# Optimization experiments

Hardware: AMD Instinct MI355X
Metric: run time of the kernel (lower is better)

## Reference

```python
import jax, jax.numpy as jnp
import numpy as np


def setup_inputs() -> dict:
    key = jax.random.key(0)
    ks = jax.random.split(key, 7)
    B, S, D, F, E = 4, 2048, 1024, 4096, 8
    scale = 0.02
    return {
        "x": jax.random.normal(ks[0], (B, S, D), dtype=jnp.float32),
        "gate_w": jax.random.normal(ks[1], (D, E), dtype=jnp.float32) * scale,
        "gate_b": jnp.zeros((E,), dtype=jnp.float32),
        "w1": jax.random.normal(ks[2], (E, D, F), dtype=jnp.float32) * scale,
        "b1": jnp.zeros((E, F), dtype=jnp.float32),
        "w2": jax.random.normal(ks[3], (E, F, D), dtype=jnp.float32) * scale,
        "b2": jnp.zeros((E, D), dtype=jnp.float32),
        "top_k": 2,
    }


def reference(x, gate_w, gate_b, w1, b1, w2, b2, top_k):
    B, S, D = x.shape
    E = w1.shape[0]
    xf = x.reshape(-1, D)                      # [T, D], T = B*S
    T = xf.shape[0]

    # Router: top-k logits, softmax over the selected k (as in torch code)
    logits = xf @ gate_w + gate_b              # [T, E]
    rw, sel = jax.lax.top_k(logits, top_k)     # [T, k], [T, k]
    w = jax.nn.softmax(rw, axis=-1)            # [T, k]

    # Dense combine weights: combine[t, e] = sum_k w[t,k] * (sel[t,k]==e)
    combine = jnp.zeros((T, E), dtype=xf.dtype)
    combine = combine.at[jnp.arange(T)[:, None], sel].add(w)

    # Loop over small fixed expert count; each expert FFN on all tokens,
    # weighted by combine (zero for unrouted tokens). Dropout p honored as 0 (eval).
    out = jnp.zeros_like(xf)
    for e in range(E):
        h = jax.nn.gelu(xf @ w1[e] + b1[e], approximate=False)  # torch F.gelu = exact
        out = out + combine[:, e:e + 1] * (h @ w2[e] + b2[e])
    return out.reshape(B, S, D)
```

## Files before the change

### kernel.cpp

```cpp
#include <hip/hip_runtime.h>
#include <math.h>

#define T_TOK 8192
#define DDIM  1024
#define FDIM  4096
#define NEXP  8
#define MT256 72
#define NSLOT (2 * T_TOK)
#define NG1   (16 * MT256)
#define NG2   (8 * MT256)

typedef __attribute__((ext_vector_type(8))) short short8;
typedef __attribute__((ext_vector_type(4))) float f32x4;
typedef unsigned short u16;
typedef unsigned int   u32;

typedef const __attribute__((address_space(1))) u32* gp_t;
typedef       __attribute__((address_space(3))) u32* lp_t;

__device__ __forceinline__ void gload16(const void* g, void* l) {
  __builtin_amdgcn_global_load_lds((gp_t)g, (lp_t)l, 16, 0, 0);
}

#define VM2 asm volatile("s_waitcnt vmcnt(2)" ::: "memory")
#define VM0 asm volatile("s_waitcnt vmcnt(0)" ::: "memory")
#define SBAR __builtin_amdgcn_s_barrier()
#define SCHED0 __builtin_amdgcn_sched_barrier(0)

__device__ __forceinline__ u16 f2bf(float f) {
  u32 u = __float_as_uint(f);
  u = u + 0x7FFFu + ((u >> 16) & 1u);
  return (u16)(u >> 16);
}

__device__ __forceinline__ int imin(int a, int b) { return a < b ? a : b; }

__device__ __forceinline__ float gelu_fast(float v) {
  float u = 0.7978845608f * (v + 0.044715f * v * v * v);
  float t2 = __expf(2.f * u);
  float th = 1.f - 2.f / (t2 + 1.f);
  return 0.5f * v * (1.f + th);
}

__device__ __forceinline__ int xcd_swz(int orig, int nwg) {
  int xcd = orig & 7;
  int q = nwg >> 3, r = nwg & 7;
  int base = (xcd < r) ? xcd * (q + 1) : r * (q + 1) + (xcd - r) * q;
  return base + (orig >> 3);
}

__global__ __launch_bounds__(256) void router_kernel(
    const float* __restrict__ x, const float* __restrict__ gw,
    const float* __restrict__ gb,
    int* __restrict__ counts, int* __restrict__ sel, float* __restrict__ wts)
{
  const int t    = blockIdx.x * 4 + (threadIdx.x >> 6);
  const int lane = threadIdx.x & 63;
  const float* xr = x + (size_t)t * DDIM;
  float lg[NEXP];
  #pragma unroll
  for (int e = 0; e < NEXP; e++) lg[e] = 0.f;
  #pragma unroll
  for (int i = 0; i < 4; i++) {
    int d0 = i * 256 + lane * 4;
    float4 v = *(const float4*)(xr + d0);
    const float* g = gw + (size_t)d0 * NEXP;
    #pragma unroll
    for (int e = 0; e < NEXP; e++)
      lg[e] += v.x * g[e] + v.y * g[NEXP + e] + v.z * g[2 * NEXP + e] + v.w * g[3 * NEXP + e];
  }
  #pragma unroll
  for (int off = 32; off > 0; off >>= 1) {
    #pragma unroll
    for (int e = 0; e < NEXP; e++) lg[e] += __shfl_down(lg[e], off);
  }
  if (lane == 0) {
    float v0 = -1e30f, v1 = -1e30f; int s0 = 0, s1 = 0;
    #pragma unroll
    for (int e = 0; e < NEXP; e++) {
      float v = lg[e] + gb[e];
      if (v > v0) { v1 = v0; s1 = s0; v0 = v; s0 = e; }
      else if (v > v1) { v1 = v; s1 = e; }
    }
    float a  = expf(v1 - v0);
    float w0 = 1.f / (1.f + a);
    sel[t * 2] = s0; sel[t * 2 + 1] = s1;
    wts[t * 2] = w0; wts[t * 2 + 1] = 1.f - w0;
    atomicAdd(&counts[s0], 1); atomicAdd(&counts[s1], 1);
  }
}

__global__ __launch_bounds__(256) void scan_assign_kernel(
    const int* __restrict__ counts, const int* __restrict__ sel,
    const float* __restrict__ wts,
    int* __restrict__ offsets, int* __restrict__ map_e, int* __restrict__ map_r,
    int* __restrict__ nT, int* __restrict__ stok, float* __restrict__ swgt)
{
  __shared__ int spos[NEXP];
  if (threadIdx.x == 0) {
    int run = 0, nt = 0;
    for (int e = 0; e < NEXP; e++) {
      offsets[e] = run; spos[e] = run;
      int c = counts[e];
      int ntile = (c + 255) >> 8;
      for (int i = 0; i < ntile; i++) { map_e[nt] = e; map_r[nt] = i * 256; nt++; }
      run += c;
    }
    nT[0] = nt;
  }
  __syncthreads();
  for (int t = threadIdx.x; t < T_TOK; t += 256) {
    #pragma unroll
    for (int k = 0; k < 2; k++) {
      int e = sel[t * 2 + k];
      int p = atomicAdd(&spos[e], 1);
      stok[p] = t; swgt[p] = wts[t * 2 + k];
    }
  }
}

__global__ __launch_bounds__(256) void xgather_kernel(
    const float* __restrict__ x, const int* __restrict__ stok,
    u16* __restrict__ Xg)
{
  const int s = blockIdx.x;
  int tok = stok[s]; if ((u32)tok >= T_TOK) tok = 0;
  float4 v = *(const float4*)(x + (size_t)tok * DDIM + threadIdx.x * 4);
  ushort4 o;
  o.x = f2bf(v.x); o.y = f2bf(v.y); o.z = f2bf(v.z); o.w = f2bf(v.w);
  *(ushort4*)(Xg + (size_t)s * DDIM + threadIdx.x * 4) = o;
}

__device__ void wtrans_tile(float* __restrict__ tile,
                            const float* __restrict__ in, u16* __restrict__ out,
                            int M, int N, int r0, int c0)
{
  const int tid = threadIdx.x;
  const int tr = tid >> 4, tc = (tid & 15) * 4;
  #pragma unroll
  for (int p = 0; p < 4; p++) {
    int r = p * 16 + tr;
    float4 v = *(const float4*)(in + (size_t)(r0 + r) * N + (c0 + tc));
    tile[r * 65 + tc]     = v.x; tile[r * 65 + tc + 1] = v.y;
    tile[r * 65 + tc + 2] = v.z; tile[r * 65 + tc + 3] = v.w;
  }
  __syncthreads();
  const int oc = tid >> 3, om = (tid & 7) * 8;
  #pragma unroll
  for (int p = 0; p < 2; p++) {
    int c = p * 32 + oc;
    short8 o;
    #pragma unroll
    for (int j = 0; j < 8; j++) o[j] = (short)f2bf(tile[(om + j) * 65 + c]);
    *(short8*)(out + (size_t)(c0 + c) * M + (r0 + om)) = o;
  }
}

__global__ __launch_bounds__(256) void wtrans_all_kernel(
    const float* __restrict__ w1, u16* __restrict__ w1t,
    const float* __restrict__ w2, u16* __restrict__ w2t)
{
  __shared__ __align__(16) float tile[64 * 65];
  const int t = blockIdx.x;
  if (t < 8192) {
    int e = t >> 10, rem = t & 1023;
    int tm = rem >> 4, tn = rem & 15;
    wtrans_tile(tile, w2 + (size_t)e * FDIM * DDIM,
                w2t + (size_t)e * FDIM * DDIM, FDIM, DDIM, tm * 64, tn * 64);
  } else {
    int tt = t - 8192;
    int e = tt >> 10, rem = tt & 1023;
    int tn = rem >> 4, tm = rem & 15;
    wtrans_tile(tile, w1 + (size_t)e * DDIM * FDIM,
                w1t + (size_t)e * DDIM * FDIM, DDIM, FDIM, tm * 64, tn * 64);
  }
}

__global__ __launch_bounds__(1024, 4) void gemm1_kernel(
    const u16* __restrict__ Xg, const u16* __restrict__ W1T,
    const float* __restrict__ B1,
    const int* __restrict__ counts, const int* __restrict__ offsets,
    const int* __restrict__ map_e, const int* __restrict__ map_r,
    const int* __restrict__ nT, u16* __restrict__ H)
{
  __shared__ __align__(16) char lds[3 * 32768];
  const int L     = xcd_swz(blockIdx.x, NG1);
  const int xg    = L / 144;
  const int local = L - xg * 144;
  const int tl    = local >> 4;
  const int n_idx = local & 15;
  const int t_idx = xg * 9 + tl;
  if (t_idx >= nT[0]) return;
  const int e    = map_e[t_idx];
  const int row0 = map_r[t_idx];
  const int cnt  = counts[e];
  const int off  = offsets[e];
  const int n0   = n_idx * 256;

  const int tid = threadIdx.x, wave = tid >> 6, lane = tid & 63;
  const int lr = lane & 15, lq = lane >> 4;
  const int wr = wave >> 2, wc = wave & 3;
  const int l2 = lane >> 2, lb = (lane & 3) * 16;

  const int R = wave * 16 + l2;
  int aidx = imin(off + row0 + R, NSLOT - 1);
  const char* gA = (const char*)Xg + (size_t)aidx * 2048 + lb;
  const char* gB = (const char*)W1T + (size_t)(e * FDIM + n0 + R) * 2048 + lb;

  auto stage = [&](int slot, int k0) {
    char* base = lds + slot * 32768;
    gload16(gA + k0, base + wave * 1024 + lane * 16);
    gload16(gB + k0, base + 16384 + wave * 1024 + lane * 16);
  };

  f32x4 acc[4][4] = {};
  auto compute = [&](int slot) {
    const u16* As = (const u16*)(lds + slot * 32768);
    const u16* Bs = (const u16*)(lds + slot * 32768 + 16384);
    short8 a[4], bf[4];
    #pragma unroll
    for (int m = 0; m < 4; m++)
      a[m] = *(const short8*)&As[(wr * 64 + m * 16 + lr) * 32 + lq * 8];
    #pragma unroll
    for (int n = 0; n < 4; n++)
      bf[n] = *(const short8*)&Bs[(wc * 64 + n * 16 + lr) * 32 + lq * 8];
    #pragma unroll
    for (int m = 0; m < 4; m++)
      #pragma unroll
      for (int n = 0; n < 4; n++)
        acc[m][n] = __builtin_amdgcn_mfma_f32_16x16x32_bf16(a[m], bf[n], acc[m][n], 0, 0, 0);
  };

  stage(0, 0); stage(1, 64);
  VM2; SCHED0; SBAR; SCHED0;
  #pragma unroll 1
  for (int t = 0; t < 32; t++) {
    if (t + 2 < 32) stage((t + 2) % 3, (t + 2) * 64);
    compute(t % 3);
    SCHED0;
    if (t + 2 < 32)       { VM2; }
    else if (t + 2 == 32) { VM0; }
    SCHED0; SBAR; SCHED0;
  }

  #pragma unroll
  for (int nn = 0; nn < 4; nn++) {
    int col = n0 + wc * 64 + nn * 16 + lr;
    float b1v = B1[e * FDIM + col];
    #pragma unroll
    for (int m = 0; m < 4; m++) {
      int rbase = wr * 64 + m * 16 + lq * 4;
      #pragma unroll
      for (int j = 0; j < 4; j++) {
        int r = rbase + j;
        if (row0 + r < cnt) {
          float v = acc[m][nn][j] + b1v;
          H[(size_t)(off + row0 + r) * FDIM + col] = f2bf(gelu_fast(v));
        }
      }
    }
  }
}

__global__ __launch_bounds__(1024, 4) void gemm2_kernel(
    const u16* __restrict__ H, const u16* __restrict__ W2T,
    const float* __restrict__ B2,
    const int* __restrict__ counts, const int* __restrict__ offsets,
    const int* __restrict__ slot_token, const float* __restrict__ slot_weight,
    const int* __restrict__ map_e, const int* __restrict__ map_r,
    const int* __restrict__ nT, float* __restrict__ out)
{
  __shared__ __align__(16) char lds[3 * 32768];
  const int L     = xcd_swz(blockIdx.x, NG2);
  const int xg    = L / 72;
  const int local = L - xg * 72;
  const int tl    = local >> 3;
  const int combo = local & 7;
  const int sp    = combo >> 2;
  const int n_idx = combo & 3;
  const int t_idx = xg * 9 + tl;
  if (t_idx >= nT[0]) return;
  const int e    = map_e[t_idx];
  const int row0 = map_r[t_idx];
  const int cnt  = counts[e];
  const int off  = offsets[e];
  const int n0   = n_idx * 256;
  const int kbase = sp * 4096;

  const int tid = threadIdx.x, wave = tid >> 6, lane = tid & 63;
  const int lr = lane & 15, lq = lane >> 4;
  const int wr = wave >> 2, wc = wave & 3;
  const int l2 = lane >> 2, lb = (lane & 3) * 16;

  const int R = wave * 16 + l2;
  int aidx = imin(off + row0 + R, NSLOT - 1);
  const char* gA = (const char*)H + (size_t)aidx * 8192 + kbase + lb;
  const char* gB = (const char*)W2T + (size_t)(e * DDIM + n0 + R) * 8192 + kbase + lb;

  auto stage = [&](int slot, int k0) {
    char* base = lds + slot * 32768;
    gload16(gA + k0, base + wave * 1024 + lane * 16);
    gload16(gB + k0, base + 16384 + wave * 1024 + lane * 16);
  };

  f32x4 acc[4][4] = {};
  auto compute = [&](int slot) {
    const u16* As = (const u16*)(lds + slot * 32768);
    const u16* Bs = (const u16*)(lds + slot * 32768 + 16384);
    short8 a[4], bf[4];
    #pragma unroll
    for (int m = 0; m < 4; m++)
      a[m] = *(const short8*)&As[(wr * 64 + m * 16 + lr) * 32 + lq * 8];
    #pragma unroll
    for (int n = 0; n < 4; n++)
      bf[n] = *(const short8*)&Bs[(wc * 64 + n * 16 + lr) * 32 + lq * 8];
    #pragma unroll
    for (int m = 0; m < 4; m++)
      #pragma unroll
      for (int n = 0; n < 4; n++)
        acc[m][n] = __builtin_amdgcn_mfma_f32_16x16x32_bf16(a[m], bf[n], acc[m][n], 0, 0, 0);
  };

  stage(0, 0); stage(1, 64);
  VM2; SCHED0; SBAR; SCHED0;
  #pragma unroll 1
  for (int t = 0; t < 64; t++) {
    if (t + 2 < 64) stage((t + 2) % 3, (t + 2) * 64);
    compute(t % 3);
    SCHED0;
    if (t + 2 < 64)       { VM2; }
    else if (t + 2 == 64) { VM0; }
    SCHED0; SBAR; SCHED0;
  }

  #pragma unroll
  for (int m = 0; m < 4; m++) {
    int rbase = wr * 64 + m * 16 + lq * 4;
    #pragma unroll
    for (int j = 0; j < 4; j++) {
      int r = rbase + j;
      if (row0 + r >= cnt) continue;
      int s = off + row0 + r;
      int tok = slot_token[s];
      float wgt = slot_weight[s];
      #pragma unroll
      for (int n = 0; n < 4; n++) {
        int col = n0 + wc * 64 + n * 16 + lr;
        float v = acc[m][n][j];
        if (sp == 0) v += B2[e * DDIM + col];
        atomicAdd(&out[(size_t)tok * DDIM + col], wgt * v);
      }
    }
  }
}

extern "C" void kernel_launch(void* const* d_in, const int* in_sizes, int n_in,
                              void* d_out, int out_size, void* d_ws, size_t ws_size,
                              hipStream_t stream)
{
  (void)in_sizes; (void)n_in; (void)ws_size;
  const float* x  = (const float*)d_in[0];
  const float* gw = (const float*)d_in[1];
  const float* gb = (const float*)d_in[2];
  const float* w1 = (const float*)d_in[3];
  const float* b1 = (const float*)d_in[4];
  const float* w2 = (const float*)d_in[5];
  const float* b2 = (const float*)d_in[6];

  char* ws = (char*)d_ws;
  int*   counts = (int*)(ws + 0);
  int*   offp   = (int*)(ws + 64);
  int*   nT     = (int*)(ws + 128);
  int*   map_e  = (int*)(ws + 256);
  int*   map_r  = (int*)(ws + 1024);

  size_t p = 2048;
  int*   sel   = (int*)(ws + p);   p += (size_t)T_TOK * 2 * 4;
  float* wts   = (float*)(ws + p); p += (size_t)T_TOK * 2 * 4;
  int*   stok  = (int*)(ws + p);   p += (size_t)NSLOT * 4;
  float* swgt  = (float*)(ws + p); p += (size_t)NSLOT * 4;
  p = (p + 1048575) & ~(size_t)1048575;
  u16*   Xg    = (u16*)(ws + p);   p += (size_t)NSLOT * DDIM * 2;
  u16*   w1t   = (u16*)(ws + p);   p += (size_t)NEXP * DDIM * FDIM * 2;
  u16*   w2t   = (u16*)(ws + p);   p += (size_t)NEXP * DDIM * FDIM * 2;
  u16*   Hbuf  = (u16*)(ws + p);

  hipMemsetAsync(ws, 0, 256, stream);
  hipMemsetAsync(d_out, 0, (size_t)out_size * sizeof(float), stream);
  router_kernel<<<T_TOK / 4, 256, 0, stream>>>(x, gw, gb, counts, sel, wts);
  scan_assign_kernel<<<1, 256, 0, stream>>>(counts, sel, wts, offp, map_e, map_r, nT, stok, swgt);
  xgather_kernel<<<NSLOT, 256, 0, stream>>>(x, stok, Xg);
  wtrans_all_kernel<<<16384, 256, 0, stream>>>(w1, w1t, w2, w2t);
  gemm1_kernel<<<NG1, 1024, 0, stream>>>(
      Xg, w1t, b1, counts, offp, map_e, map_r, nT, Hbuf);
  gemm2_kernel<<<NG2, 1024, 0, stream>>>(
      Hbuf, w2t, b2, counts, offp, stok, swgt, map_e, map_r, nT, (float*)d_out);
}
```

Before: 834.4 us.

## Deepen GEMM LDS pipeline to four stages and XOR-swizzle LDS layout

Both expert GEMM kernels move from a 3-slot to a 4-slot LDS ring buffer, so loads are prefetched three k-steps ahead, and the vmcnt waits are adjusted to match. The 16-byte chunks within each 64-byte LDS row are XOR-swizzled by row index, on the global source offset and on the MFMA fragment reads, to cut LDS bank conflicts. LDS per block grows from 96KB to 128KB, which may limit co-residency, though with 1024-thread blocks only one block likely fits per CU in either case.

Result: no change. 837.5 us (+0.4%).

```diff
diff --git a/kernel.cpp b/kernel.cpp
--- a/kernel.cpp
+++ b/kernel.cpp
@@ -22,6 +22,7 @@
   __builtin_amdgcn_global_load_lds((gp_t)g, (lp_t)l, 16, 0, 0);
 }
 
+#define VM4 asm volatile("s_waitcnt vmcnt(4)" ::: "memory")
 #define VM2 asm volatile("s_waitcnt vmcnt(2)" ::: "memory")
 #define VM0 asm volatile("s_waitcnt vmcnt(0)" ::: "memory")
 #define SBAR __builtin_amdgcn_s_barrier()
@@ -183,7 +184,7 @@
     const int* __restrict__ map_e, const int* __restrict__ map_r,
     const int* __restrict__ nT, u16* __restrict__ H)
 {
-  __shared__ __align__(16) char lds[3 * 32768];
+  __shared__ __align__(16) char lds[4 * 32768];
   const int L     = xcd_swz(blockIdx.x, NG1);
   const int xg    = L / 144;
   const int local = L - xg * 144;
@@ -200,12 +201,13 @@
   const int tid = threadIdx.x, wave = tid >> 6, lane = tid & 63;
   const int lr = lane & 15, lq = lane >> 4;
   const int wr = wave >> 2, wc = wave & 3;
-  const int l2 = lane >> 2, lb = (lane & 3) * 16;
+  const int l2 = lane >> 2;
+  const int usrc = ((lane & 3) ^ (l2 & 3)) * 16;
 
   const int R = wave * 16 + l2;
   int aidx = imin(off + row0 + R, NSLOT - 1);
-  const char* gA = (const char*)Xg + (size_t)aidx * 2048 + lb;
-  const char* gB = (const char*)W1T + (size_t)(e * FDIM + n0 + R) * 2048 + lb;
+  const char* gA = (const char*)Xg + (size_t)aidx * 2048 + usrc;
+  const char* gB = (const char*)W1T + (size_t)(e * FDIM + n0 + R) * 2048 + usrc;
 
   auto stage = [&](int slot, int k0) {
     char* base = lds + slot * 32768;
@@ -217,13 +219,14 @@
   auto compute = [&](int slot) {
     const u16* As = (const u16*)(lds + slot * 32768);
     const u16* Bs = (const u16*)(lds + slot * 32768 + 16384);
+    const int ua = (lq ^ (lr & 3)) * 8;
     short8 a[4], bf[4];
     #pragma unroll
     for (int m = 0; m < 4; m++)
-      a[m] = *(const short8*)&As[(wr * 64 + m * 16 + lr) * 32 + lq * 8];
+      a[m] = *(const short8*)&As[(wr * 64 + m * 16 + lr) * 32 + ua];
     #pragma unroll
     for (int n = 0; n < 4; n++)
-      bf[n] = *(const short8*)&Bs[(wc * 64 + n * 16 + lr) * 32 + lq * 8];
+      bf[n] = *(const short8*)&Bs[(wc * 64 + n * 16 + lr) * 32 + ua];
     #pragma unroll
     for (int m = 0; m < 4; m++)
       #pragma unroll
@@ -231,14 +234,15 @@
         acc[m][n] = __builtin_amdgcn_mfma_f32_16x16x32_bf16(a[m], bf[n], acc[m][n], 0, 0, 0);
   };
 
-  stage(0, 0); stage(1, 64);
-  VM2; SCHED0; SBAR; SCHED0;
+  stage(0, 0); stage(1, 64); stage(2, 128);
+  VM4; SCHED0; SBAR; SCHED0;
   #pragma unroll 1
   for (int t = 0; t < 32; t++) {
-    if (t + 2 < 32) stage((t + 2) % 3, (t + 2) * 64);
-    compute(t % 3);
+    if (t + 3 < 32) stage((t + 3) & 3, (t + 3) * 64);
+    compute(t & 3);
     SCHED0;
-    if (t + 2 < 32)       { VM2; }
+    if (t + 3 < 32)       { VM4; }
+    else if (t + 3 == 32) { VM2; }
     else if (t + 2 == 32) { VM0; }
     SCHED0; SBAR; SCHED0;
   }
@@ -270,7 +274,7 @@
     const int* __restrict__ map_e, const int* __restrict__ map_r,
     const int* __restrict__ nT, float* __restrict__ out)
 {
-  __shared__ __align__(16) char lds[3 * 32768];
+  __shared__ __align__(16) char lds[4 * 32768];
   const int L     = xcd_swz(blockIdx.x, NG2);
   const int xg    = L / 72;
   const int local = L - xg * 72;
@@ -290,12 +294,13 @@
   const int tid = threadIdx.x, wave = tid >> 6, lane = tid & 63;
   const int lr = lane & 15, lq = lane >> 4;
   const int wr = wave >> 2, wc = wave & 3;
-  const int l2 = lane >> 2, lb = (lane & 3) * 16;
+  const int l2 = lane >> 2;
+  const int usrc = ((lane & 3) ^ (l2 & 3)) * 16;
 
   const int R = wave * 16 + l2;
   int aidx = imin(off + row0 + R, NSLOT - 1);
-  const char* gA = (const char*)H + (size_t)aidx * 8192 + kbase + lb;
-  const char* gB = (const char*)W2T + (size_t)(e * DDIM + n0 + R) * 8192 + kbase + lb;
+  const char* gA = (const char*)H + (size_t)aidx * 8192 + kbase + usrc;
+  const char* gB = (const char*)W2T + (size_t)(e * DDIM + n0 + R) * 8192 + kbase + usrc;
 
   auto stage = [&](int slot, int k0) {
     char* base = lds + slot * 32768;
@@ -307,13 +312,14 @@
   auto compute = [&](int slot) {
     const u16* As = (const u16*)(lds + slot * 32768);
     const u16* Bs = (const u16*)(lds + slot * 32768 + 16384);
+    const int ua = (lq ^ (lr & 3)) * 8;
     short8 a[4], bf[4];
     #pragma unroll
     for (int m = 0; m < 4; m++)
-      a[m] = *(const short8*)&As[(wr * 64 + m * 16 + lr) * 32 + lq * 8];
+      a[m] = *(const short8*)&As[(wr * 64 + m * 16 + lr) * 32 + ua];
     #pragma unroll
     for (int n = 0; n < 4; n++)
-      bf[n] = *(const short8*)&Bs[(wc * 64 + n * 16 + lr) * 32 + lq * 8];
+      bf[n] = *(const short8*)&Bs[(wc * 64 + n * 16 + lr) * 32 + ua];
     #pragma unroll
     for (int m = 0; m < 4; m++)
       #pragma unroll
@@ -321,14 +327,15 @@
         acc[m][n] = __builtin_amdgcn_mfma_f32_16x16x32_bf16(a[m], bf[n], acc[m][n], 0, 0, 0);
   };
 
-  stage(0, 0); stage(1, 64);
-  VM2; SCHED0; SBAR; SCHED0;
+  stage(0, 0); stage(1, 64); stage(2, 128);
+  VM4; SCHED0; SBAR; SCHED0;
   #pragma unroll 1
   for (int t = 0; t < 64; t++) {
-    if (t + 2 < 64) stage((t + 2) % 3, (t + 2) * 64);
-    compute(t % 3);
+    if (t + 3 < 64) stage((t + 3) & 3, (t + 3) * 64);
+    compute(t & 3);
     SCHED0;
-    if (t + 2 < 64)       { VM2; }
+    if (t + 3 < 64)       { VM4; }
+    else if (t + 3 == 64) { VM2; }
     else if (t + 2 == 64) { VM0; }
     SCHED0; SBAR; SCHED0;
   }
```

## Fuse router, bf16 cast and weight transpose; gather tokens inside gemm1

Applied to the files above, without the earlier changes.

Merges the router and the weight-transpose kernels into one prep kernel that also writes a bf16 copy of x per token. The separate xgather pass that materialised a per-slot bf16 copy of x is removed. gemm1 now reads A rows indirectly through the slot-to-token map. The scan kernel is widened to 1024 threads. This drops one launch and roughly halves the bf16 x traffic, at the cost of scattered row addresses in gemm1's A loads.

After: 780.2 us. 1.07x faster.

```diff
diff --git a/kernel.cpp b/kernel.cpp
--- a/kernel.cpp
+++ b/kernel.cpp
@@ -49,14 +49,59 @@
   return base + (orig >> 3);
 }
 
-__global__ __launch_bounds__(256) void router_kernel(
+__device__ void wtrans_tile(float* __restrict__ tile,
+                            const float* __restrict__ in, u16* __restrict__ out,
+                            int M, int N, int r0, int c0)
+{
+  const int tid = threadIdx.x;
+  const int tr = tid >> 4, tc = (tid & 15) * 4;
+  #pragma unroll
+  for (int p = 0; p < 4; p++) {
+    int r = p * 16 + tr;
+    float4 v = *(const float4*)(in + (size_t)(r0 + r) * N + (c0 + tc));
+    tile[r * 65 + tc]     = v.x; tile[r * 65 + tc + 1] = v.y;
+    tile[r * 65 + tc + 2] = v.z; tile[r * 65 + tc + 3] = v.w;
+  }
+  __syncthreads();
+  const int oc = tid >> 3, om = (tid & 7) * 8;
+  #pragma unroll
+  for (int p = 0; p < 2; p++) {
+    int c = p * 32 + oc;
+    short8 o;
+    #pragma unroll
+    for (int j = 0; j < 8; j++) o[j] = (short)f2bf(tile[(om + j) * 65 + c]);
+    *(short8*)(out + (size_t)(c0 + c) * M + (r0 + om)) = o;
+  }
+}
+
+__global__ __launch_bounds__(256) void prep_kernel(
     const float* __restrict__ x, const float* __restrict__ gw,
-    const float* __restrict__ gb,
-    int* __restrict__ counts, int* __restrict__ sel, float* __restrict__ wts)
-{
-  const int t    = blockIdx.x * 4 + (threadIdx.x >> 6);
+    const float* __restrict__ gb, u16* __restrict__ xb,
+    int* __restrict__ counts, int* __restrict__ sel, float* __restrict__ wts,
+    const float* __restrict__ w1, u16* __restrict__ w1t,
+    const float* __restrict__ w2, u16* __restrict__ w2t)
+{
+  __shared__ __align__(16) float tile[64 * 65];
+  const int b = blockIdx.x;
+  if (b < 16384) {
+    if (b < 8192) {
+      int e = b >> 10, rem = b & 1023;
+      int tm = rem >> 4, tn = rem & 15;
+      wtrans_tile(tile, w2 + (size_t)e * FDIM * DDIM,
+                  w2t + (size_t)e * FDIM * DDIM, FDIM, DDIM, tm * 64, tn * 64);
+    } else {
+      int tt = b - 8192;
+      int e = tt >> 10, rem = tt & 1023;
+      int tn = rem >> 4, tm = rem & 15;
+      wtrans_tile(tile, w1 + (size_t)e * DDIM * FDIM,
+                  w1t + (size_t)e * DDIM * FDIM, DDIM, FDIM, tm * 64, tn * 64);
+    }
+    return;
+  }
+  const int t    = (b - 16384) * 4 + (threadIdx.x >> 6);
   const int lane = threadIdx.x & 63;
   const float* xr = x + (size_t)t * DDIM;
+  u16* xbr = xb + (size_t)t * DDIM;
   float lg[NEXP];
   #pragma unroll
   for (int e = 0; e < NEXP; e++) lg[e] = 0.f;
@@ -64,6 +109,9 @@
   for (int i = 0; i < 4; i++) {
     int d0 = i * 256 + lane * 4;
     float4 v = *(const float4*)(xr + d0);
+    ushort4 o;
+    o.x = f2bf(v.x); o.y = f2bf(v.y); o.z = f2bf(v.z); o.w = f2bf(v.w);
+    *(ushort4*)(xbr + d0) = o;
     const float* g = gw + (size_t)d0 * NEXP;
     #pragma unroll
     for (int e = 0; e < NEXP; e++)
@@ -90,7 +138,7 @@
   }
 }
 
-__global__ __launch_bounds__(256) void scan_assign_kernel(
+__global__ __launch_bounds__(1024) void scan_assign_kernel(
     const int* __restrict__ counts, const int* __restrict__ sel,
     const float* __restrict__ wts,
     int* __restrict__ offsets, int* __restrict__ map_e, int* __restrict__ map_r,
@@ -109,7 +157,7 @@
     nT[0] = nt;
   }
   __syncthreads();
-  for (int t = threadIdx.x; t < T_TOK; t += 256) {
+  for (int t = threadIdx.x; t < T_TOK; t += 1024) {
     #pragma unroll
     for (int k = 0; k < 2; k++) {
       int e = sel[t * 2 + k];
@@ -119,66 +167,9 @@
   }
 }
 
-__global__ __launch_bounds__(256) void xgather_kernel(
-    const float* __restrict__ x, const int* __restrict__ stok,
-    u16* __restrict__ Xg)
-{
-  const int s = blockIdx.x;
-  int tok = stok[s]; if ((u32)tok >= T_TOK) tok = 0;
-  float4 v = *(const float4*)(x + (size_t)tok * DDIM + threadIdx.x * 4);
-  ushort4 o;
-  o.x = f2bf(v.x); o.y = f2bf(v.y); o.z = f2bf(v.z); o.w = f2bf(v.w);
-  *(ushort4*)(Xg + (size_t)s * DDIM + threadIdx.x * 4) = o;
-}
-
-__device__ void wtrans_tile(float* __restrict__ tile,
-                            const float* __restrict__ in, u16* __restrict__ out,
-                            int M, int N, int r0, int c0)
-{
-  const int tid = threadIdx.x;
-  const int tr = tid >> 4, tc = (tid & 15) * 4;
-  #pragma unroll
-  for (int p = 0; p < 4; p++) {
-    int r = p * 16 + tr;
-    float4 v = *(const float4*)(in + (size_t)(r0 + r) * N + (c0 + tc));
-    tile[r * 65 + tc]     = v.x; tile[r * 65 + tc + 1] = v.y;
-    tile[r * 65 + tc + 2] = v.z; tile[r * 65 + tc + 3] = v.w;
-  }
-  __syncthreads();
-  const int oc = tid >> 3, om = (tid & 7) * 8;
-  #pragma unroll
-  for (int p = 0; p < 2; p++) {
-    int c = p * 32 + oc;
-    short8 o;
-    #pragma unroll
-    for (int j = 0; j < 8; j++) o[j] = (short)f2bf(tile[(om + j) * 65 + c]);
-    *(short8*)(out + (size_t)(c0 + c) * M + (r0 + om)) = o;
-  }
-}
-
-__global__ __launch_bounds__(256) void wtrans_all_kernel(
-    const float* __restrict__ w1, u16* __restrict__ w1t,
-    const float* __restrict__ w2, u16* __restrict__ w2t)
-{
-  __shared__ __align__(16) float tile[64 * 65];
-  const int t = blockIdx.x;
-  if (t < 8192) {
-    int e = t >> 10, rem = t & 1023;
-    int tm = rem >> 4, tn = rem & 15;
-    wtrans_tile(tile, w2 + (size_t)e * FDIM * DDIM,
-                w2t + (size_t)e * FDIM * DDIM, FDIM, DDIM, tm * 64, tn * 64);
-  } else {
-    int tt = t - 8192;
-    int e = tt >> 10, rem = tt & 1023;
-    int tn = rem >> 4, tm = rem & 15;
-    wtrans_tile(tile, w1 + (size_t)e * DDIM * FDIM,
-                w1t + (size_t)e * DDIM * FDIM, DDIM, FDIM, tm * 64, tn * 64);
-  }
-}
-
 __global__ __launch_bounds__(1024, 4) void gemm1_kernel(
-    const u16* __restrict__ Xg, const u16* __restrict__ W1T,
-    const float* __restrict__ B1,
+    const u16* __restrict__ xb, const int* __restrict__ slot_token,
+    const u16* __restrict__ W1T, const float* __restrict__ B1,
     const int* __restrict__ counts, const int* __restrict__ offsets,
     const int* __restrict__ map_e, const int* __restrict__ map_r,
     const int* __restrict__ nT, u16* __restrict__ H)
@@ -203,8 +194,9 @@
   const int l2 = lane >> 2, lb = (lane & 3) * 16;
 
   const int R = wave * 16 + l2;
-  int aidx = imin(off + row0 + R, NSLOT - 1);
-  const char* gA = (const char*)Xg + (size_t)aidx * 2048 + lb;
+  int tok = slot_token[imin(off + row0 + R, NSLOT - 1)];
+  if ((u32)tok >= T_TOK) tok = 0;
+  const char* gA = (const char*)xb + (size_t)tok * 2048 + lb;
   const char* gB = (const char*)W1T + (size_t)(e * FDIM + n0 + R) * 2048 + lb;
 
   auto stage = [&](int slot, int k0) {
@@ -380,19 +372,18 @@
   int*   stok  = (int*)(ws + p);   p += (size_t)NSLOT * 4;
   float* swgt  = (float*)(ws + p); p += (size_t)NSLOT * 4;
   p = (p + 1048575) & ~(size_t)1048575;
-  u16*   Xg    = (u16*)(ws + p);   p += (size_t)NSLOT * DDIM * 2;
+  u16*   xb    = (u16*)(ws + p);   p += (size_t)T_TOK * DDIM * 2;
   u16*   w1t   = (u16*)(ws + p);   p += (size_t)NEXP * DDIM * FDIM * 2;
   u16*   w2t   = (u16*)(ws + p);   p += (size_t)NEXP * DDIM * FDIM * 2;
   u16*   Hbuf  = (u16*)(ws + p);
 
   hipMemsetAsync(ws, 0, 256, stream);
   hipMemsetAsync(d_out, 0, (size_t)out_size * sizeof(float), stream);
-  router_kernel<<<T_TOK / 4, 256, 0, stream>>>(x, gw, gb, counts, sel, wts);
-  scan_assign_kernel<<<1, 256, 0, stream>>>(counts, sel, wts, offp, map_e, map_r, nT, stok, swgt);
-  xgather_kernel<<<NSLOT, 256, 0, stream>>>(x, stok, Xg);
-  wtrans_all_kernel<<<16384, 256, 0, stream>>>(w1, w1t, w2, w2t);
+  prep_kernel<<<16384 + T_TOK / 4, 256, 0, stream>>>(
+      x, gw, gb, xb, counts, sel, wts, w1, w1t, w2, w2t);
+  scan_assign_kernel<<<1, 1024, 0, stream>>>(counts, sel, wts, offp, map_e, map_r, nT, stok, swgt);
   gemm1_kernel<<<NG1, 1024, 0, stream>>>(
-      Xg, w1t, b1, counts, offp, map_e, map_r, nT, Hbuf);
+      xb, stok, w1t, b1, counts, offp, map_e, map_r, nT, Hbuf);
   gemm2_kernel<<<NG2, 1024, 0, stream>>>(
       Hbuf, w2t, b2, counts, offp, stok, swgt, map_e, map_r, nT, (float*)d_out);
 }
```
